# Optimization experiments

Hardware: AMD Instinct MI355X
Metric: run time of the kernel (lower is better)

Reference implementation:

```python
import jax, jax.numpy as jnp
import numpy as np

EMB = 1024
NHEADS = 16
HEAD_DIM = EMB // NHEADS


def setup_inputs() -> dict:
    key = jax.random.key(0)
    k_x, k_wa, k_ba, k_wp, k_bp = jax.random.split(key, 5)
    x = jax.random.normal(k_x, (4, 2048, EMB), dtype=jnp.float32)
    # HF Conv1D: y = x @ W + b, W shape (in_features, out_features)
    w_attn = jax.random.normal(k_wa, (EMB, 3 * EMB), dtype=jnp.float32) * 0.02
    b_attn = jnp.zeros((3 * EMB,), dtype=jnp.float32)
    w_proj = jax.random.normal(k_wp, (EMB, EMB), dtype=jnp.float32) * 0.02
    b_proj = jnp.zeros((EMB,), dtype=jnp.float32)
    return {"x": x, "w_attn": w_attn, "b_attn": b_attn, "w_proj": w_proj, "b_proj": b_proj}


def reference(x, w_attn, b_attn, w_proj, b_proj):
    B, T, E = x.shape
    H, D = NHEADS, HEAD_DIM
    qkv = x @ w_attn + b_attn                      # [B, T, 3E]
    q, k, v = jnp.split(qkv, 3, axis=-1)           # each [B, T, E]
    # split heads -> [B, H, T, D]
    q = q.reshape(B, T, H, D).transpose(0, 2, 1, 3)
    k = k.reshape(B, T, H, D).transpose(0, 2, 1, 3)
    v = v.reshape(B, T, H, D).transpose(0, 2, 1, 3)
    # attention: explicit scores, scaled by sqrt(head_dim); NO causal mask (as in source)
    scores = jnp.einsum('bhqd,bhkd->bhqk', q, k) / jnp.sqrt(jnp.asarray(D, x.dtype))
    probs = jax.nn.softmax(scores, axis=-1)
    a = jnp.einsum('bhqk,bhkd->bhqd', probs, v)    # [B, H, T, D]
    a = a.transpose(0, 2, 1, 3).reshape(B, T, E)   # merge heads
    return a @ w_proj + b_proj
```

## Files before the change

### kernel.cpp

```cpp
#include <hip/hip_runtime.h>
#include <hip/hip_bf16.h>

#define EMB 1024
#define THREE_EMB 3072
#define T_SEQ 2048
#define NB 4
#define NH 16
#define HD 64
#define MROWS 8192
#define NBH 64

#define QSCALE 0.18033688011112042f

typedef _Float16 half8 __attribute__((ext_vector_type(8)));
typedef _Float16 half4v __attribute__((ext_vector_type(4)));
typedef float f32x4v __attribute__((ext_vector_type(4)));
typedef unsigned u32x2 __attribute__((ext_vector_type(2)));

static __device__ __forceinline__ f32x4v mfma16(half8 a, half8 b, f32x4v c) {
  return __builtin_amdgcn_mfma_f32_16x16x32_f16(a, b, c, 0, 0, 0);
}

static __device__ __forceinline__ void gload16(const void* g, void* l) {
  __builtin_amdgcn_global_load_lds(
      (const __attribute__((address_space(1))) void*)g,
      (__attribute__((address_space(3))) void*)l, 16, 0, 0);
}

static __device__ __forceinline__ half8 mk_half8(unsigned a, unsigned b,
                                                 unsigned c, unsigned d) {
  union {
    unsigned w[4];
    half8 h;
  } u;
  u.w[0] = a; u.w[1] = b; u.w[2] = c; u.w[3] = d;
  return u.h;
}

static __device__ __forceinline__ unsigned pk16(float a, float b) {
  auto e = __builtin_amdgcn_cvt_pkrtz(a, b);
  unsigned r;
  __builtin_memcpy(&r, &e, 4);
  return r;
}

__global__ __launch_bounds__(256) void cast_x(const float* __restrict__ X,
                                              _Float16* __restrict__ H) {
  const size_t i = ((size_t)blockIdx.x * 256 + threadIdx.x) * 8;
  const float4 a = *(const float4*)&X[i];
  const float4 b = *(const float4*)&X[i + 4];
  const float va[8] = {a.x, a.y, a.z, a.w, b.x, b.y, b.z, b.w};
  half8 h;
#pragma unroll
  for (int j = 0; j < 8; ++j) h[j] = (_Float16)va[j];
  *(half8*)&H[i] = h;
}

__global__ __launch_bounds__(256) void tsplit_w(const float* __restrict__ W,
                                                _Float16* __restrict__ Th,
                                                int N) {
  __shared__ float tile[32][33];
  const int tid = threadIdx.x;
  const int k0 = blockIdx.x * 32;
  const int n0 = blockIdx.y * 32;
  const int c = tid & 31;
  const int r4 = (tid >> 5) * 4;
#pragma unroll
  for (int rr = 0; rr < 4; ++rr)
    tile[r4 + rr][c] = W[(size_t)(k0 + r4 + rr) * N + n0 + c];
  __syncthreads();
#pragma unroll
  for (int rr = 0; rr < 4; ++rr)
    Th[(size_t)(n0 + r4 + rr) * EMB + k0 + c] = (_Float16)tile[c][r4 + rr];
}

template <int MODE>
__global__ __launch_bounds__(256) void mfma_gemm(
    const _Float16* __restrict__ Ah, const _Float16* __restrict__ Bh,
    const float* __restrict__ bias, float* __restrict__ OutF,
    _Float16* __restrict__ Qh, _Float16* __restrict__ Kh,
    _Float16* __restrict__ Vt) {
  __shared__ __align__(16) _Float16 SAh[128 * 64];
  __shared__ __align__(16) _Float16 SBh[128 * 64];

  const int tid = threadIdx.x;
  const int wv = tid >> 6;
  const int lane = tid & 63;
  const int l15 = lane & 15;
  const int lhi = lane >> 4;
  const int wm = wv >> 1, wn = wv & 1;
  const int m0 = blockIdx.x * 128;
  const int n0 = blockIdx.y * 128;

  const int rl = lane >> 3;
  const int cs8 = ((lane & 7) ^ rl) * 8;
  const _Float16* gA0 = Ah + (size_t)(m0 + rl) * EMB + cs8;
  const _Float16* gB0 = Bh + (size_t)(n0 + rl) * EMB + cs8;

  f32x4v acc[4][4];
#pragma unroll
  for (int mi = 0; mi < 4; ++mi)
#pragma unroll
    for (int ni = 0; ni < 4; ++ni) acc[mi][ni] = (f32x4v){0.f, 0.f, 0.f, 0.f};

  const int sb0 = ((lhi) ^ (l15 & 7)) * 8;
  const int sb1 = ((4 + lhi) ^ (l15 & 7)) * 8;

  for (int k0 = 0; k0 < EMB; k0 += 64) {
    __syncthreads();
    {
      const int i0 = (wv & 1) * 8;
      if (wv < 2) {
#pragma unroll
        for (int i = 0; i < 8; ++i)
          gload16(gA0 + k0 + (size_t)(i0 + i) * 8 * EMB, &SAh[(i0 + i) * 512]);
      } else {
#pragma unroll
        for (int i = 0; i < 8; ++i)
          gload16(gB0 + k0 + (size_t)(i0 + i) * 8 * EMB, &SBh[(i0 + i) * 512]);
      }
    }
    __syncthreads();
#pragma unroll
    for (int kk = 0; kk < 2; ++kk) {
      const int sb = kk ? sb1 : sb0;
      half8 am[4], bn[4];
#pragma unroll
      for (int mi = 0; mi < 4; ++mi) {
        const int r = wm * 64 + mi * 16 + l15;
        am[mi] = *(const half8*)&SAh[r * 64 + sb];
      }
#pragma unroll
      for (int ni = 0; ni < 4; ++ni) {
        const int r = wn * 64 + ni * 16 + l15;
        bn[ni] = *(const half8*)&SBh[r * 64 + sb];
      }
      __builtin_amdgcn_s_setprio(1);
#pragma unroll
      for (int mi = 0; mi < 4; ++mi)
#pragma unroll
        for (int ni = 0; ni < 4; ++ni)
          acc[mi][ni] = mfma16(am[mi], bn[ni], acc[mi][ni]);
      __builtin_amdgcn_s_setprio(0);
    }
  }

  const int gmB = m0 + wm * 64 + lhi * 4;
  const int gnB = n0 + wn * 64 + l15;
  if (MODE == 1) {
#pragma unroll
    for (int mi = 0; mi < 4; ++mi)
#pragma unroll
      for (int ni = 0; ni < 4; ++ni) {
        const int gn = gnB + ni * 16;
        const float bi = bias[gn];
#pragma unroll
        for (int r = 0; r < 4; ++r) {
          const int gm = gmB + mi * 16 + r;
          OutF[(size_t)gm * EMB + gn] = acc[mi][ni][r] + bi;
        }
      }
  } else {
    const int which = n0 >> 10;
#pragma unroll
    for (int mi = 0; mi < 4; ++mi) {
#pragma unroll
      for (int ni = 0; ni < 4; ++ni) {
        const int gn = gnB + ni * 16;
        const float bi = bias[gn];
        const int d = gn & 63;
        const int h = (gn >> 6) & 15;
        const int gm0 = gmB + mi * 16;
        const int b = gm0 >> 11;
        const int t0 = gm0 & 2047;
        const int bh = b * NH + h;
        if (which == 2) {
          half4v hv;
#pragma unroll
          for (int r = 0; r < 4; ++r) hv[r] = (_Float16)(acc[mi][ni][r] + bi);
          *(half4v*)&Vt[((size_t)bh * HD + d) * T_SEQ + t0] = hv;
        } else if (which == 1) {
#pragma unroll
          for (int r = 0; r < 4; ++r) {
            const float v = acc[mi][ni][r] + bi;
            Kh[((size_t)bh * T_SEQ + t0 + r) * HD + d] = (_Float16)v;
          }
        } else {
#pragma unroll
          for (int r = 0; r < 4; ++r) {
            const float v = (acc[mi][ni][r] + bi) * QSCALE;
            Qh[((size_t)bh * T_SEQ + t0 + r) * HD + d] = (_Float16)v;
          }
        }
      }
    }
  }
}

__global__ __launch_bounds__(256) void attn_kernel(
    const _Float16* __restrict__ Qh, const _Float16* __restrict__ Kh,
    const _Float16* __restrict__ Vt, _Float16* __restrict__ AO) {
  __shared__ __align__(16) _Float16 KhS[2][64 * 64];
  __shared__ __align__(16) _Float16 VtS[2][64 * 64];

  const int tid = threadIdx.x;
  const int w = tid >> 6;
  const int lane = tid & 63;
  const int l15 = lane & 15;
  const int lhi = lane >> 4;
  const int sw = l15 & 7;

  const int bid = blockIdx.x;
  const int idx = bid >> 3;
  const int bh = (bid & 7) * 8 + (idx & 7);
  const int qb = idx >> 3;
  const int q0 = qb * 256 + w * 64;
  const int b = bh >> 4;
  const int h = bh & 15;

  half8 qh[4][2];
#pragma unroll
  for (int qf = 0; qf < 4; ++qf) {
    const size_t qbase =
        ((size_t)bh * T_SEQ + q0 + qf * 16 + l15) * HD + lhi * 8;
#pragma unroll
    for (int m2 = 0; m2 < 2; ++m2)
      qh[qf][m2] = *(const half8*)&Qh[qbase + m2 * 32];
  }

  half8 ones;
#pragma unroll
  for (int j = 0; j < 8; ++j) ones[j] = (_Float16)1.0f;

  f32x4v O[4][4];
  float l[4] = {0.f, 0.f, 0.f, 0.f};
#pragma unroll
  for (int qf = 0; qf < 4; ++qf)
#pragma unroll
    for (int c = 0; c < 4; ++c) O[qf][c] = (f32x4v){0.f, 0.f, 0.f, 0.f};

  const int so = lane >> 3;
  const int schunk = ((lane & 7) ^ so) * 8;
  const size_t kgb = (size_t)bh * T_SEQ * HD;
  const size_t vgb = (size_t)bh * HD * T_SEQ;
  const int rb = w * 16;

#define STAGE(buf, kt_)                                              \
  {                                                                  \
    _Pragma("unroll") for (int i = 0; i < 2; ++i) {                  \
      const int row = rb + i * 8 + so;                               \
      gload16(Kh + kgb + (size_t)((kt_) + row) * HD + schunk,        \
              &KhS[(buf)][(rb + i * 8) * 64]);                       \
      gload16(Vt + vgb + (size_t)row * T_SEQ + (kt_) + schunk,       \
              &VtS[(buf)][(rb + i * 8) * 64]);                       \
    }                                                                \
  }

  STAGE(0, 0);
  int cur = 0;

  for (int kt = 0; kt < T_SEQ; kt += 64) {
    asm volatile("s_waitcnt vmcnt(0)" ::: "memory");
    __builtin_amdgcn_s_barrier();
    __builtin_amdgcn_sched_barrier(0);
    if (kt + 64 < T_SEQ) STAGE(cur ^ 1, kt + 64);

    f32x4v s[4][4];
    __builtin_amdgcn_s_setprio(1);
#pragma unroll
    for (int c = 0; c < 4; ++c) {
      const int krow = c * 16 + l15;
      const half8 k0 = *(const half8*)&KhS[cur][krow * 64 + (lhi ^ sw) * 8];
      const half8 k1 =
          *(const half8*)&KhS[cur][krow * 64 + ((4 + lhi) ^ sw) * 8];
#pragma unroll
      for (int qf = 0; qf < 4; ++qf) {
        f32x4v t = (f32x4v){0.f, 0.f, 0.f, 0.f};
        t = mfma16(k0, qh[qf][0], t);
        t = mfma16(k1, qh[qf][1], t);
        s[qf][c] = t;
      }
    }
    __builtin_amdgcn_s_setprio(0);

    half8 vv[4][2];
#pragma unroll
    for (int c = 0; c < 4; ++c) {
      const int vrow = c * 16 + l15;
      vv[c][0] = *(const half8*)&VtS[cur][vrow * 64 + (lhi ^ sw) * 8];
      vv[c][1] = *(const half8*)&VtS[cur][vrow * 64 + ((4 + lhi) ^ sw) * 8];
    }

#pragma unroll
    for (int qf = 0; qf < 4; ++qf) {
      unsigned u[4][2];
#pragma unroll
      for (int c = 0; c < 4; ++c) {
        const float p0 = __builtin_amdgcn_exp2f(s[qf][c][0]);
        const float p1 = __builtin_amdgcn_exp2f(s[qf][c][1]);
        const float p2 = __builtin_amdgcn_exp2f(s[qf][c][2]);
        const float p3 = __builtin_amdgcn_exp2f(s[qf][c][3]);
        u[c][0] = pk16(p0, p1);
        u[c][1] = pk16(p2, p3);
      }
      unsigned w0[4], w1[4];
#pragma unroll
      for (int X = 0; X < 2; ++X) {
#pragma unroll
        for (int hh = 0; hh < 2; ++hh) {
          const u32x2 o = __builtin_amdgcn_permlane32_swap(
              u[2 * X][hh], u[2 * X + 1][hh], false, false);
          const u32x2 W =
              __builtin_amdgcn_permlane16_swap(o[0], o[1], false, false);
          if (X == 0) {
            w0[hh] = W[0];
            w0[2 + hh] = W[1];
          } else {
            w1[hh] = W[0];
            w1[2 + hh] = W[1];
          }
        }
      }
      const half8 pb0 = mk_half8(w0[0], w0[1], w0[2], w0[3]);
      const half8 pb1 = mk_half8(w1[0], w1[1], w1[2], w1[3]);

      f32x4v ls = (f32x4v){0.f, 0.f, 0.f, 0.f};
      ls = mfma16(ones, pb0, ls);
      ls = mfma16(ones, pb1, ls);
      __builtin_amdgcn_s_setprio(1);
#pragma unroll
      for (int c = 0; c < 4; ++c) {
        O[qf][c] = mfma16(vv[c][0], pb0, O[qf][c]);
        O[qf][c] = mfma16(vv[c][1], pb1, O[qf][c]);
      }
      __builtin_amdgcn_s_setprio(0);
      l[qf] += ls[0];
    }
    cur ^= 1;
  }

#pragma unroll
  for (int qf = 0; qf < 4; ++qf) {
    const float inv = 1.0f / l[qf];
    const size_t rowb =
        (size_t)(b * T_SEQ + q0 + qf * 16 + l15) * EMB + h * HD + lhi * 4;
#pragma unroll
    for (int c = 0; c < 4; ++c) {
      half4v hv;
#pragma unroll
      for (int r = 0; r < 4; ++r) hv[r] = (_Float16)(O[qf][c][r] * inv);
      *(half4v*)&AO[rowb + c * 16] = hv;
    }
  }
#undef STAGE
}

extern "C" void kernel_launch(void* const* d_in, const int* in_sizes, int n_in,
                              void* d_out, int out_size, void* d_ws,
                              size_t ws_size, hipStream_t stream) {
  const float* x = (const float*)d_in[0];
  const float* w_attn = (const float*)d_in[1];
  const float* b_attn = (const float*)d_in[2];
  const float* w_proj = (const float*)d_in[3];
  const float* b_proj = (const float*)d_in[4];
  float* out = (float*)d_out;

  const size_t SZX = (size_t)MROWS * EMB;
  const size_t SZWA = (size_t)THREE_EMB * EMB;
  const size_t SZWP = (size_t)EMB * EMB;

  _Float16* Xh = (_Float16*)d_ws;
  _Float16* WaH = Xh + SZX;
  _Float16* WpH = WaH + SZWA;
  _Float16* Qh = WpH + SZWP;
  _Float16* Kh = Qh + SZX;
  _Float16* Vt = Kh + SZX;
  _Float16* AO = Xh;

  cast_x<<<4096, 256, 0, stream>>>(x, Xh);
  tsplit_w<<<dim3(32, 96), 256, 0, stream>>>(w_attn, WaH, THREE_EMB);
  tsplit_w<<<dim3(32, 32), 256, 0, stream>>>(w_proj, WpH, EMB);

  mfma_gemm<0><<<dim3(64, 24), 256, 0, stream>>>(Xh, WaH, b_attn, nullptr, Qh,
                                                 Kh, Vt);
  attn_kernel<<<dim3(512), 256, 0, stream>>>(Qh, Kh, Vt, AO);
  mfma_gemm<1><<<dim3(64, 8), 256, 0, stream>>>(AO, WpH, b_proj, out, nullptr,
                                                nullptr, nullptr);
}
```

Measured before the change: 188.7 us.

## Split attention key range across two wave groups per block with LDS reduction

Doubles the attention block to 512 threads. Two groups of four waves each process half of the key sequence for the same 256 queries, each with its own double-buffered K/V shared tiles. At the end the partial O accumulators and row sums are combined through LDS before normalising and writing out. This raises the number of waves available to hide latency with the same grid, at the cost of more LDS, more registers per block and an extra reduction with several barriers. Softmax has no max subtraction, so partial sums add directly.

```diff
diff --git a/kernel.cpp b/kernel.cpp
--- a/kernel.cpp
+++ b/kernel.cpp
@@ -197,14 +197,16 @@
   }
 }
 
-__global__ __launch_bounds__(256) void attn_kernel(
+__global__ __launch_bounds__(512) void attn_kernel(
     const _Float16* __restrict__ Qh, const _Float16* __restrict__ Kh,
     const _Float16* __restrict__ Vt, _Float16* __restrict__ AO) {
-  __shared__ __align__(16) _Float16 KhS[2][64 * 64];
-  __shared__ __align__(16) _Float16 VtS[2][64 * 64];
+  __shared__ __align__(16) _Float16 KhS[2][2][64 * 64];
+  __shared__ __align__(16) _Float16 VtS[2][2][64 * 64];
 
   const int tid = threadIdx.x;
   const int w = tid >> 6;
+  const int grp = w >> 2;
+  const int wl = w & 3;
   const int lane = tid & 63;
   const int l15 = lane & 15;
   const int lhi = lane >> 4;
@@ -214,7 +216,7 @@
   const int idx = bid >> 3;
   const int bh = (bid & 7) * 8 + (idx & 7);
   const int qb = idx >> 3;
-  const int q0 = qb * 256 + w * 64;
+  const int q0 = qb * 256 + wl * 64;
   const int b = bh >> 4;
   const int h = bh & 15;
 
@@ -243,36 +245,39 @@
   const int schunk = ((lane & 7) ^ so) * 8;
   const size_t kgb = (size_t)bh * T_SEQ * HD;
   const size_t vgb = (size_t)bh * HD * T_SEQ;
-  const int rb = w * 16;
+  const int rb = wl * 16;
 
 #define STAGE(buf, kt_)                                              \
   {                                                                  \
     _Pragma("unroll") for (int i = 0; i < 2; ++i) {                  \
       const int row = rb + i * 8 + so;                               \
       gload16(Kh + kgb + (size_t)((kt_) + row) * HD + schunk,        \
-              &KhS[(buf)][(rb + i * 8) * 64]);                       \
+              &KhS[grp][(buf)][(rb + i * 8) * 64]);                  \
       gload16(Vt + vgb + (size_t)row * T_SEQ + (kt_) + schunk,       \
-              &VtS[(buf)][(rb + i * 8) * 64]);                       \
+              &VtS[grp][(buf)][(rb + i * 8) * 64]);                  \
     }                                                                \
   }
 
-  STAGE(0, 0);
+  const int kt0 = grp * 1024;
+  const int ktEnd = kt0 + 1024;
+  STAGE(0, kt0);
   int cur = 0;
 
-  for (int kt = 0; kt < T_SEQ; kt += 64) {
+  for (int kt = kt0; kt < ktEnd; kt += 64) {
     asm volatile("s_waitcnt vmcnt(0)" ::: "memory");
     __builtin_amdgcn_s_barrier();
     __builtin_amdgcn_sched_barrier(0);
-    if (kt + 64 < T_SEQ) STAGE(cur ^ 1, kt + 64);
+    if (kt + 64 < ktEnd) STAGE(cur ^ 1, kt + 64);
 
     f32x4v s[4][4];
     __builtin_amdgcn_s_setprio(1);
 #pragma unroll
     for (int c = 0; c < 4; ++c) {
       const int krow = c * 16 + l15;
-      const half8 k0 = *(const half8*)&KhS[cur][krow * 64 + (lhi ^ sw) * 8];
+      const half8 k0 =
+          *(const half8*)&KhS[grp][cur][krow * 64 + (lhi ^ sw) * 8];
       const half8 k1 =
-          *(const half8*)&KhS[cur][krow * 64 + ((4 + lhi) ^ sw) * 8];
+          *(const half8*)&KhS[grp][cur][krow * 64 + ((4 + lhi) ^ sw) * 8];
 #pragma unroll
       for (int qf = 0; qf < 4; ++qf) {
         f32x4v t = (f32x4v){0.f, 0.f, 0.f, 0.f};
@@ -287,8 +292,9 @@
 #pragma unroll
     for (int c = 0; c < 4; ++c) {
       const int vrow = c * 16 + l15;
-      vv[c][0] = *(const half8*)&VtS[cur][vrow * 64 + (lhi ^ sw) * 8];
-      vv[c][1] = *(const half8*)&VtS[cur][vrow * 64 + ((4 + lhi) ^ sw) * 8];
+      vv[c][0] = *(const half8*)&VtS[grp][cur][vrow * 64 + (lhi ^ sw) * 8];
+      vv[c][1] =
+          *(const half8*)&VtS[grp][cur][vrow * 64 + ((4 + lhi) ^ sw) * 8];
     }
 
 #pragma unroll
@@ -339,17 +345,43 @@
     cur ^= 1;
   }
 
+  float* scr = (float*)&KhS[0][0][0];
+  __syncthreads();
 #pragma unroll
   for (int qf = 0; qf < 4; ++qf) {
-    const float inv = 1.0f / l[qf];
-    const size_t rowb =
-        (size_t)(b * T_SEQ + q0 + qf * 16 + l15) * EMB + h * HD + lhi * 4;
-#pragma unroll
-    for (int c = 0; c < 4; ++c) {
-      half4v hv;
-#pragma unroll
-      for (int r = 0; r < 4; ++r) hv[r] = (_Float16)(O[qf][c][r] * inv);
-      *(half4v*)&AO[rowb + c * 16] = hv;
+    if (w >= 4) {
+      float* dst = scr + ((size_t)((w - 4) * 64 + lane)) * 17;
+#pragma unroll
+      for (int c = 0; c < 4; ++c)
+#pragma unroll
+        for (int r = 0; r < 4; ++r) dst[c * 4 + r] = O[qf][c][r];
+      dst[16] = l[qf];
+    }
+    __syncthreads();
+    if (w < 4) {
+      const float* src = scr + ((size_t)(w * 64 + lane)) * 17;
+#pragma unroll
+      for (int c = 0; c < 4; ++c)
+#pragma unroll
+        for (int r = 0; r < 4; ++r) O[qf][c][r] += src[c * 4 + r];
+      l[qf] += src[16];
+    }
+    __syncthreads();
+  }
+
+  if (w < 4) {
+#pragma unroll
+    for (int qf = 0; qf < 4; ++qf) {
+      const float inv = 1.0f / l[qf];
+      const size_t rowb =
+          (size_t)(b * T_SEQ + q0 + qf * 16 + l15) * EMB + h * HD + lhi * 4;
+#pragma unroll
+      for (int c = 0; c < 4; ++c) {
+        half4v hv;
+#pragma unroll
+        for (int r = 0; r < 4; ++r) hv[r] = (_Float16)(O[qf][c][r] * inv);
+        *(half4v*)&AO[rowb + c * 16] = hv;
+      }
     }
   }
 #undef STAGE
@@ -383,7 +415,7 @@
 
   mfma_gemm<0><<<dim3(64, 24), 256, 0, stream>>>(Xh, WaH, b_attn, nullptr, Qh,
                                                  Kh, Vt);
-  attn_kernel<<<dim3(512), 256, 0, stream>>>(Qh, Kh, Vt, AO);
+  attn_kernel<<<dim3(512), 512, 0, stream>>>(Qh, Kh, Vt, AO);
   mfma_gemm<1><<<dim3(64, 8), 256, 0, stream>>>(AO, WpH, b_proj, out, nullptr,
                                                 nullptr, nullptr);
 }
```

Measured after the change: 190.7 us. Within noise of the previous version (+1.1%).
